# Kernel optimization log

Hardware: AMD Instinct MI355X
Metric: run time of the kernel (lower is better)

Reference implementation:

```python
import jax, jax.numpy as jnp
import numpy as np

IN_FEATURES = 4096
OUT_FEATURES = 14336
TOKENS = 32


def setup_inputs() -> dict:
    key = jax.random.key(0)
    k1, k2, k3 = jax.random.split(key, 3)
    x = jax.random.normal(k1, (TOKENS, IN_FEATURES), dtype=jnp.float32)
    # int8-valued quantized weight stored as int32 (symmetric Q8, range [-127, 127])
    weight = jax.random.randint(k2, (OUT_FEATURES, IN_FEATURES), -127, 128, dtype=jnp.int32)
    # per-in-feature (per-column of [out,in] matrix) positive scales
    scales = jax.random.uniform(k3, (IN_FEATURES,), dtype=jnp.float32, minval=0.001, maxval=0.02)
    return {"x": x, "weight": weight, "scales": scales}


def reference(x, weight, scales):
    # Original torch: dequant[o,i] = weight[o,i] * scales[i]; out = x @ dequant.T
    # Equivalent fused form: out[t,o] = sum_i (x[t,i]*scales[i]) * weight[o,i]
    x_scaled = x * scales[None, :]            # [T, in]
    w = weight.astype(jnp.float32)            # [out, in]
    out = jnp.einsum('ti,oi->to', x_scaled, w)  # [T, out]
    return out
```

## Files before the change

### kernel.cpp

```cpp
#include <hip/hip_runtime.h>
#include <stdint.h>
#include <stddef.h>

#define IN_F   4096
#define OUT_F  14336
#define TOK    32

#define OTILE  64
#define ISPLIT 16
#define IBLK   (IN_F / ISPLIT)
#define ICHUNK 64
#define NCHUNK (IBLK / ICHUNK)
#define KBPB   (IBLK / 32)

typedef const __attribute__((address_space(1))) void* gas_ptr;
typedef __attribute__((address_space(3))) void* las_ptr;
typedef __attribute__((ext_vector_type(8))) short bf16x8;
typedef __attribute__((ext_vector_type(4))) float f32x4;

__global__ __launch_bounds__(256) void prep_kernel(
    const float* __restrict__ x, const float* __restrict__ scales,
    int4* __restrict__ xfrag, float* __restrict__ out)
{
    const int f = blockIdx.x * 256 + threadIdx.x;
    if (f < (TOK * IN_F / 8)) {
        const int t  = f >> 9;
        const int i8 = f & 511;
        const int kb = i8 >> 2;
        const int kg = i8 & 3;
        const float4* xp = (const float4*)(x + (size_t)t * IN_F + i8 * 8);
        const float4* sp = (const float4*)(scales + i8 * 8);
        float4 x0 = xp[0], x1 = xp[1];
        float4 s0 = sp[0], s1 = sp[1];
        float v[8] = { x0.x*s0.x, x0.y*s0.y, x0.z*s0.z, x0.w*s0.w,
                       x1.x*s1.x, x1.y*s1.y, x1.z*s1.z, x1.w*s1.w };
        uint32_t h[8];
#pragma unroll
        for (int j = 0; j < 8; ++j) {
            uint32_t b = __float_as_uint(v[j]);
            b += 0x7fffu + ((b >> 16) & 1u);
            h[j] = b >> 16;
        }
        int4 d;
        d.x = (int)(h[0] | (h[1] << 16));
        d.y = (int)(h[2] | (h[3] << 16));
        d.z = (int)(h[4] | (h[5] << 16));
        d.w = (int)(h[6] | (h[7] << 16));
        xfrag[((kb * 2 + (t >> 4)) * 64) + kg * 16 + (t & 15)] = d;
    }
    if (f < (OUT_F * TOK / 4)) {
        ((float4*)out)[f] = make_float4(0.f, 0.f, 0.f, 0.f);
    }
}

__global__ __launch_bounds__(256, 4) void qgemm_kernel(
    const int* __restrict__ wgt, const int4* __restrict__ xfrag,
    float* __restrict__ out)
{
    __shared__ int wtile[2][OTILE * ICHUNK];
    const int lane = threadIdx.x & 63;
    const int wv   = threadIdx.x >> 6;
    const int wvu  = __builtin_amdgcn_readfirstlane(wv);
    const int o0   = blockIdx.x * OTILE;
    const int ib0  = blockIdx.y * IBLK;
    const int lx   = lane & 15;
    const int quad = lane >> 4;

    int4 a[KBPB][2];
#pragma unroll
    for (int kb = 0; kb < KBPB; ++kb)
#pragma unroll
        for (int mt = 0; mt < 2; ++mt)
            a[kb][mt] = xfrag[((blockIdx.y * KBPB + kb) * 2 + mt) * 64 + lane];

    auto stage = [&](int buf, int c) {
#pragma unroll
        for (int k = 0; k < 4; ++k) {
            const int m = wvu * 4 + k;
            const int r = m * 4 + (lane >> 4);
            const int j = lx ^ (r & 15);
            const int* g = wgt + (size_t)(o0 + r) * IN_F
                               + (ib0 + c * ICHUNK) + (j << 2);
            int* l = &wtile[buf][m * 256];
            __builtin_amdgcn_global_load_lds((gas_ptr)g, (las_ptr)l, 16, 0, 0);
        }
    };

    f32x4 acc[2] = { {0.f,0.f,0.f,0.f}, {0.f,0.f,0.f,0.f} };

    stage(0, 0);
    __syncthreads();

    int cur = 0;
#pragma unroll
    for (int c = 0; c < NCHUNK; ++c) {
        if (c + 1 < NCHUNK) stage(cur ^ 1, c + 1);

        const int* rowp = &wtile[cur][(wvu * 16 + lx) * ICHUNK];
#pragma unroll
        for (int kb2 = 0; kb2 < 2; ++kb2) {
            const int g0 = kb2 * 8 + quad * 2;
            const int4 w0 = *(const int4*)(rowp + ((g0 ^ lx) << 2));
            const int4 w1 = *(const int4*)(rowp + (((g0 + 1) ^ lx) << 2));
            bf16x8 b;
            b[0] = (short)(__float_as_uint((float)w0.x) >> 16);
            b[1] = (short)(__float_as_uint((float)w0.y) >> 16);
            b[2] = (short)(__float_as_uint((float)w0.z) >> 16);
            b[3] = (short)(__float_as_uint((float)w0.w) >> 16);
            b[4] = (short)(__float_as_uint((float)w1.x) >> 16);
            b[5] = (short)(__float_as_uint((float)w1.y) >> 16);
            b[6] = (short)(__float_as_uint((float)w1.z) >> 16);
            b[7] = (short)(__float_as_uint((float)w1.w) >> 16);
            const int kbl = c * 2 + kb2;
            bf16x8 a0, a1;
            __builtin_memcpy(&a0, &a[kbl][0], 16);
            __builtin_memcpy(&a1, &a[kbl][1], 16);
            acc[0] = __builtin_amdgcn_mfma_f32_16x16x32_bf16(a0, b, acc[0], 0, 0, 0);
            acc[1] = __builtin_amdgcn_mfma_f32_16x16x32_bf16(a1, b, acc[1], 0, 0, 0);
        }
        __syncthreads();
        cur ^= 1;
    }

#pragma unroll
    for (int mt = 0; mt < 2; ++mt)
#pragma unroll
        for (int reg = 0; reg < 4; ++reg) {
            const int t = mt * 16 + quad * 4 + reg;
            atomicAdd(&out[(size_t)t * OUT_F + o0 + wvu * 16 + lx], acc[mt][reg]);
        }
}

extern "C" void kernel_launch(void* const* d_in, const int* in_sizes, int n_in,
                              void* d_out, int out_size, void* d_ws, size_t ws_size,
                              hipStream_t stream)
{
    const float* x      = (const float*)d_in[0];
    const int*   wgt    = (const int*)d_in[1];
    const float* scales = (const float*)d_in[2];
    float* out = (float*)d_out;
    int4*  xfrag = (int4*)d_ws;

    prep_kernel<<<dim3((TOK * IN_F) / 256), 256, 0, stream>>>(x, scales, xfrag, out);

    dim3 grid(OUT_F / OTILE, ISPLIT);
    qgemm_kernel<<<grid, 256, 0, stream>>>(wgt, xfrag, out);
}
```

Before: 328.5 us.

## Load weights directly from global memory into registers, dropping LDS staging

Replaces the double-buffered global_load_lds staging of weight tiles with direct per-lane vector loads from global memory into registers, fully unrolled over the K block. This removes the LDS traffic and the per-chunk barriers, and lets all weight loads be issued early for more memory-level parallelism. In exchange, each load instruction touches 16 different rows, so coalescing is weaker, and register pressure rises.

```diff
diff --git a/kernel.cpp b/kernel.cpp
--- a/kernel.cpp
+++ b/kernel.cpp
@@ -9,12 +9,8 @@
 #define OTILE  64
 #define ISPLIT 16
 #define IBLK   (IN_F / ISPLIT)
-#define ICHUNK 64
-#define NCHUNK (IBLK / ICHUNK)
 #define KBPB   (IBLK / 32)
 
-typedef const __attribute__((address_space(1))) void* gas_ptr;
-typedef __attribute__((address_space(3))) void* las_ptr;
 typedef __attribute__((ext_vector_type(8))) short bf16x8;
 typedef __attribute__((ext_vector_type(4))) float f32x4;
 
@@ -57,14 +53,12 @@
     const int* __restrict__ wgt, const int4* __restrict__ xfrag,
     float* __restrict__ out)
 {
-    __shared__ int wtile[2][OTILE * ICHUNK];
     const int lane = threadIdx.x & 63;
     const int wv   = threadIdx.x >> 6;
-    const int wvu  = __builtin_amdgcn_readfirstlane(wv);
-    const int o0   = blockIdx.x * OTILE;
-    const int ib0  = blockIdx.y * IBLK;
     const int lx   = lane & 15;
     const int quad = lane >> 4;
+    const int ob   = blockIdx.x * OTILE + wv * 16;
+    const int ib0  = blockIdx.y * IBLK;
 
     int4 a[KBPB][2];
 #pragma unroll
@@ -73,53 +67,28 @@
         for (int mt = 0; mt < 2; ++mt)
             a[kb][mt] = xfrag[((blockIdx.y * KBPB + kb) * 2 + mt) * 64 + lane];
 
-    auto stage = [&](int buf, int c) {
-#pragma unroll
-        for (int k = 0; k < 4; ++k) {
-            const int m = wvu * 4 + k;
-            const int r = m * 4 + (lane >> 4);
-            const int j = lx ^ (r & 15);
-            const int* g = wgt + (size_t)(o0 + r) * IN_F
-                               + (ib0 + c * ICHUNK) + (j << 2);
-            int* l = &wtile[buf][m * 256];
-            __builtin_amdgcn_global_load_lds((gas_ptr)g, (las_ptr)l, 16, 0, 0);
-        }
-    };
-
     f32x4 acc[2] = { {0.f,0.f,0.f,0.f}, {0.f,0.f,0.f,0.f} };
 
-    stage(0, 0);
-    __syncthreads();
+    const int* wp = wgt + (size_t)(ob + lx) * IN_F + ib0 + quad * 8;
 
-    int cur = 0;
 #pragma unroll
-    for (int c = 0; c < NCHUNK; ++c) {
-        if (c + 1 < NCHUNK) stage(cur ^ 1, c + 1);
-
-        const int* rowp = &wtile[cur][(wvu * 16 + lx) * ICHUNK];
-#pragma unroll
-        for (int kb2 = 0; kb2 < 2; ++kb2) {
-            const int g0 = kb2 * 8 + quad * 2;
-            const int4 w0 = *(const int4*)(rowp + ((g0 ^ lx) << 2));
-            const int4 w1 = *(const int4*)(rowp + (((g0 + 1) ^ lx) << 2));
-            bf16x8 b;
-            b[0] = (short)(__float_as_uint((float)w0.x) >> 16);
-            b[1] = (short)(__float_as_uint((float)w0.y) >> 16);
-            b[2] = (short)(__float_as_uint((float)w0.z) >> 16);
-            b[3] = (short)(__float_as_uint((float)w0.w) >> 16);
-            b[4] = (short)(__float_as_uint((float)w1.x) >> 16);
-            b[5] = (short)(__float_as_uint((float)w1.y) >> 16);
-            b[6] = (short)(__float_as_uint((float)w1.z) >> 16);
-            b[7] = (short)(__float_as_uint((float)w1.w) >> 16);
-            const int kbl = c * 2 + kb2;
-            bf16x8 a0, a1;
-            __builtin_memcpy(&a0, &a[kbl][0], 16);
-            __builtin_memcpy(&a1, &a[kbl][1], 16);
-            acc[0] = __builtin_amdgcn_mfma_f32_16x16x32_bf16(a0, b, acc[0], 0, 0, 0);
-            acc[1] = __builtin_amdgcn_mfma_f32_16x16x32_bf16(a1, b, acc[1], 0, 0, 0);
-        }
-        __syncthreads();
-        cur ^= 1;
+    for (int kb = 0; kb < KBPB; ++kb) {
+        const int4 w0 = *(const int4*)(wp + kb * 32);
+        const int4 w1 = *(const int4*)(wp + kb * 32 + 4);
+        bf16x8 b;
+        b[0] = (short)(__float_as_uint((float)w0.x) >> 16);
+        b[1] = (short)(__float_as_uint((float)w0.y) >> 16);
+        b[2] = (short)(__float_as_uint((float)w0.z) >> 16);
+        b[3] = (short)(__float_as_uint((float)w0.w) >> 16);
+        b[4] = (short)(__float_as_uint((float)w1.x) >> 16);
+        b[5] = (short)(__float_as_uint((float)w1.y) >> 16);
+        b[6] = (short)(__float_as_uint((float)w1.z) >> 16);
+        b[7] = (short)(__float_as_uint((float)w1.w) >> 16);
+        bf16x8 a0, a1;
+        __builtin_memcpy(&a0, &a[kb][0], 16);
+        __builtin_memcpy(&a1, &a[kb][1], 16);
+        acc[0] = __builtin_amdgcn_mfma_f32_16x16x32_bf16(a0, b, acc[0], 0, 0, 0);
+        acc[1] = __builtin_amdgcn_mfma_f32_16x16x32_bf16(a1, b, acc[1], 0, 0, 0);
     }
 
 #pragma unroll
@@ -127,7 +96,7 @@
 #pragma unroll
         for (int reg = 0; reg < 4; ++reg) {
             const int t = mt * 16 + quad * 4 + reg;
-            atomicAdd(&out[(size_t)t * OUT_F + o0 + wvu * 16 + lx], acc[mt][reg]);
+            atomicAdd(&out[(size_t)t * OUT_F + ob + lx], acc[mt][reg]);
         }
 }
 
```

Result: no change. 331.6 us (+1.0%).
